# Optimization experiments

Hardware: AMD Instinct MI355X
Metric: run time of the kernel (lower is better)

## Reference

```python
import jax, jax.numpy as jnp
import numpy as np

N, E, F_IN, H = 10000, 20000, 128, 8
C1, C2 = 512, 256          # per-head channels: head_dim1*8, head_dim2*8
B, OUT = 64, 10            # graphs per batch, output_dim


def _lin(k, fi, fo):
    return (jax.random.normal(k, (fi, fo), jnp.float32) / np.sqrt(fi)).astype(jnp.float32)


def setup_inputs() -> dict:
    key = jax.random.key(0)
    ks = jax.random.split(key, 24)
    inp = {
        "x": jax.random.normal(ks[0], (N, F_IN), jnp.float32),
        "edge_index": jax.random.randint(ks[1], (2, E), 0, N),
        "batch": jnp.sort(jax.random.randint(ks[2], (N,), 0, B)),
        # conv1 (in=F_IN, per-head C1, H heads)
        "Wq1": _lin(ks[3], F_IN, H * C1), "bq1": 0.01 * jax.random.normal(ks[4], (H * C1,)),
        "Wk1": _lin(ks[5], F_IN, H * C1), "bk1": 0.01 * jax.random.normal(ks[6], (H * C1,)),
        "Wv1": _lin(ks[7], F_IN, H * C1), "bv1": 0.01 * jax.random.normal(ks[8], (H * C1,)),
        "Ws1": _lin(ks[9], F_IN, C1), "bs1": 0.01 * jax.random.normal(ks[10], (C1,)),
        # conv2 (in=C1, per-head C2)
        "Wq2": _lin(ks[11], C1, H * C2), "bq2": 0.01 * jax.random.normal(ks[12], (H * C2,)),
        "Wk2": _lin(ks[13], C1, H * C2), "bk2": 0.01 * jax.random.normal(ks[14], (H * C2,)),
        "Wv2": _lin(ks[15], C1, H * C2), "bv2": 0.01 * jax.random.normal(ks[16], (H * C2,)),
        "Ws2": _lin(ks[17], C1, C2), "bs2": 0.01 * jax.random.normal(ks[18], (C2,)),
        # GlobalAttention gate and final fc
        "Wg": _lin(ks[19], C2, 1), "bg": jnp.zeros((1,), jnp.float32),
        "Wf": _lin(ks[20], C2, OUT), "bf": 0.01 * jax.random.normal(ks[21], (OUT,)),
    }
    return inp


def _segment_softmax(alpha, idx, n):
    # numerically-stable softmax over variable-size segments (PyG softmax)
    amax = jax.ops.segment_max(alpha, idx, num_segments=n)
    amax = jnp.where(jnp.isfinite(amax), amax, 0.0)
    e = jnp.exp(alpha - amax[idx])
    denom = jax.ops.segment_sum(e, idx, num_segments=n)
    return e / (denom[idx] + 1e-16)


def _transformer_conv(x, edge_index, Wq, bq, Wk, bk, Wv, bv, Ws, bs, C):
    n = x.shape[0]
    src, dst = edge_index[0], edge_index[1]  # message flows src -> dst
    q = (x @ Wq + bq).reshape(n, H, C)
    k = (x @ Wk + bk).reshape(n, H, C)
    v = (x @ Wv + bv).reshape(n, H, C)
    # per-edge multi-head attention logits [E, H]
    alpha = jnp.einsum('ehc,ehc->eh', q[dst], k[src]) / np.sqrt(C).astype(np.float32)
    a = _segment_softmax(alpha, dst, n)                       # [E, H]
    out = jax.ops.segment_sum(a[:, :, None] * v[src], dst, num_segments=n)  # [N, H, C]
    out = out.mean(axis=1)                                    # concat=False -> head mean
    return out + x @ Ws + bs                                  # root/skip connection


def reference(x, edge_index, batch,
              Wq1, bq1, Wk1, bk1, Wv1, bv1, Ws1, bs1,
              Wq2, bq2, Wk2, bk2, Wv2, bv2, Ws2, bs2,
              Wg, bg, Wf, bf):
    h = jax.nn.elu(_transformer_conv(x, edge_index, Wq1, bq1, Wk1, bk1, Wv1, bv1, Ws1, bs1, C1))
    h = jax.nn.elu(_transformer_conv(h, edge_index, Wq2, bq2, Wk2, bk2, Wv2, bv2, Ws2, bs2, C2))
    # GlobalAttention pooling: gate softmax within each graph, weighted sum
    gate = _segment_softmax((h @ Wg + bg)[:, 0], batch, B)    # [N]
    g = jax.ops.segment_sum(gate[:, None] * h, batch, num_segments=B)  # [B, C2]
    return g @ Wf + bf
```

## Files before the change

### kernel.cpp

```cpp
#include <hip/hip_runtime.h>
#include <math.h>

#define NN 10000
#define NE 20000
#define FIN 128
#define NHEAD 8
#define C1 512
#define C2 256
#define NB 64
#define NOUT 10

typedef _Float16 half8v __attribute__((ext_vector_type(8)));
typedef _Float16 half4v __attribute__((ext_vector_type(4)));
typedef _Float16 half2v __attribute__((ext_vector_type(2)));
typedef float f32x4 __attribute__((ext_vector_type(4)));

template<int VEC> struct VecT;
template<> struct VecT<2> { using T = half2v; };
template<> struct VecT<4> { using T = half4v; };
template<> struct VecT<8> { using T = half8v; };

__device__ __forceinline__ unsigned enc_f(float f) {
    unsigned u = __float_as_uint(f);
    return (u & 0x80000000u) ? ~u : (u | 0x80000000u);
}
__device__ __forceinline__ float dec_f(unsigned e) {
    return (e & 0x80000000u) ? __uint_as_float(e & 0x7fffffffu) : __uint_as_float(~e);
}

__device__ __forceinline__ void gload16(const _Float16* g, _Float16* l) {
    __builtin_amdgcn_global_load_lds(
        (const __attribute__((address_space(1))) unsigned int*)(const void*)g,
        (__attribute__((address_space(3))) unsigned int*)(void*)l, 16, 0, 0);
}

__device__ __forceinline__ void swz_map(int nwg, int gx, int SW, int& bx, int& by) {
    int orig = blockIdx.x;
    int q = nwg >> 3, r = nwg & 7;
    int xcd = orig & 7, lid = orig >> 3;
    int wgid = (xcd < r ? xcd * (q + 1) : r * (q + 1) + (xcd - r) * q) + lid;
    int gy = nwg / gx;
    int sh = SW * gy;
    int stripe = wgid / sh;
    int rem = wgid - stripe * sh;
    int byq = rem / SW;
    by = byq;
    bx = stripe * SW + (rem - byq * SW);
}

__global__ void cvt_f16(const float* __restrict__ in, _Float16* __restrict__ out, int n) {
    int i = blockIdx.x * blockDim.x + threadIdx.x;
    if (i < n) out[i] = (_Float16)in[i];
}

__global__ void transpose_cvt(const float* __restrict__ W, _Float16* __restrict__ Wt,
                              int K, int N) {
    __shared__ float tile[32][33];
    int n0 = blockIdx.x * 32, k0 = blockIdx.y * 32;
    int tx = threadIdx.x, ty = threadIdx.y;
    for (int j = ty; j < 32; j += 8) tile[j][tx] = W[(size_t)(k0 + j) * N + n0 + tx];
    __syncthreads();
    for (int j = ty; j < 32; j += 8)
        Wt[(size_t)(n0 + j) * K + k0 + tx] = (_Float16)tile[tx][j];
}

__global__ void transpose_stack(const float* __restrict__ Wv, _Float16* __restrict__ Bt,
                                int Cin, int Cout) {
    __shared__ float tile[32][33];
    int h = blockIdx.z;
    int c0 = blockIdx.x * 32, k0 = blockIdx.y * 32;
    int tx = threadIdx.x, ty = threadIdx.y;
    for (int j = ty; j < 32; j += 8)
        tile[j][tx] = Wv[(size_t)(k0 + j) * (NHEAD * Cout) + (size_t)h * Cout + c0 + tx];
    __syncthreads();
    for (int j = ty; j < 32; j += 8)
        Bt[(size_t)(c0 + j) * (NHEAD * Cin) + (size_t)h * Cin + k0 + tx] = (_Float16)tile[tx][j];
}

__global__ void bvmean_k(const float* __restrict__ bv, float* __restrict__ bvm, int C) {
    int c = blockIdx.x * blockDim.x + threadIdx.x;
    if (c >= C) return;
    float s = 0.f;
    #pragma unroll
    for (int h = 0; h < NHEAD; ++h) s += bv[h * C + c];
    bvm[c] = s * (1.0f / NHEAD);
}

__global__ void bcat2_k(const float* __restrict__ bq2, const float* __restrict__ bk2,
                        const float* __restrict__ bv2, const float* __restrict__ bs2,
                        float* __restrict__ o) {
    int i = blockIdx.x * blockDim.x + threadIdx.x;
    const int n = NHEAD * C2;
    if (i < n) o[i] = bq2[i];
    else if (i < 2 * n) o[i] = bk2[i - n];
    else if (i < 3 * n) o[i] = bv2[i - 2 * n];
    else if (i < 3 * n + C2) o[i] = bs2[i - 3 * n];
}

__global__ void mstack_k(const _Float16* __restrict__ wtq1, const _Float16* __restrict__ wtk1,
                         _Float16* __restrict__ Mst) {
    int h = blockIdx.z;
    int i = blockIdx.x * 16 + threadIdx.x;
    int j = blockIdx.y * 16 + threadIdx.y;
    float acc = 0.f;
    for (int c = 0; c < C1; ++c)
        acc += (float)wtq1[((size_t)h * C1 + c) * FIN + i] *
               (float)wtk1[((size_t)h * C1 + c) * FIN + j];
    Mst[((size_t)h * FIN + j) * FIN + i] = (_Float16)acc;
}

__global__ void uvprep_w(const float* __restrict__ Wq1, const float* __restrict__ Wk1,
                         const float* __restrict__ bq1, const float* __restrict__ bk1,
                         float* __restrict__ u, float* __restrict__ v) {
    int wid = (blockIdx.x * blockDim.x + threadIdx.x) >> 6;
    int lane = threadIdx.x & 63;
    if (wid >= NHEAD * FIN) return;
    int h = wid >> 7, i = wid & 127;
    const float* wq = Wq1 + (size_t)i * (NHEAD * C1) + h * C1;
    const float* wk = Wk1 + (size_t)i * (NHEAD * C1) + h * C1;
    const float* bk = bk1 + h * C1;
    const float* bq = bq1 + h * C1;
    int c = lane * 8;
    float4 a0 = *(const float4*)(wq + c),  a1 = *(const float4*)(wq + c + 4);
    float4 p0 = *(const float4*)(bk + c),  p1 = *(const float4*)(bk + c + 4);
    float4 b0 = *(const float4*)(wk + c),  b1 = *(const float4*)(wk + c + 4);
    float4 q0 = *(const float4*)(bq + c),  q1 = *(const float4*)(bq + c + 4);
    float su = a0.x*p0.x + a0.y*p0.y + a0.z*p0.z + a0.w*p0.w
             + a1.x*p1.x + a1.y*p1.y + a1.z*p1.z + a1.w*p1.w;
    float sv = b0.x*q0.x + b0.y*q0.y + b0.z*q0.z + b0.w*q0.w
             + b1.x*q1.x + b1.y*q1.y + b1.z*q1.z + b1.w*q1.w;
    #pragma unroll
    for (int off = 32; off; off >>= 1) {
        su += __shfl_xor(su, off);
        sv += __shfl_xor(sv, off);
    }
    if (lane == 0) { u[h * FIN + i] = su; v[h * FIN + i] = sv; }
}

__global__ void chd_k(const float* __restrict__ bq1, const float* __restrict__ bk1,
                      float* __restrict__ ch) {
    int h = threadIdx.x >> 6, lane = threadIdx.x & 63;
    int c = lane * 8;
    const float* bq = bq1 + h * C1;
    const float* bk = bk1 + h * C1;
    float4 a0 = *(const float4*)(bq + c), a1 = *(const float4*)(bq + c + 4);
    float4 b0 = *(const float4*)(bk + c), b1 = *(const float4*)(bk + c + 4);
    float s = a0.x*b0.x + a0.y*b0.y + a0.z*b0.z + a0.w*b0.w
            + a1.x*b1.x + a1.y*b1.y + a1.z*b1.z + a1.w*b1.w;
    #pragma unroll
    for (int off = 32; off; off >>= 1) s += __shfl_xor(s, off);
    if (lane == 0) ch[h] = s;
}

__global__ void udvs_w(const _Float16* __restrict__ xb, const float* __restrict__ u,
                       const float* __restrict__ v, const float* __restrict__ ch,
                       float* __restrict__ ud, float* __restrict__ vs) {
    int n = (blockIdx.x * blockDim.x + threadIdx.x) >> 6;
    int lane = threadIdx.x & 63;
    if (n >= NN) return;
    half2v xv = *(const half2v*)(xb + (size_t)n * FIN + lane * 2);
    float x0 = (float)xv[0], x1 = (float)xv[1];
    #pragma unroll
    for (int h = 0; h < NHEAD; ++h) {
        float2 uu = *(const float2*)(u + h * FIN + lane * 2);
        float2 vv = *(const float2*)(v + h * FIN + lane * 2);
        float su = x0 * uu.x + x1 * uu.y;
        float sv = x0 * vv.x + x1 * vv.y;
        #pragma unroll
        for (int off = 32; off; off >>= 1) {
            su += __shfl_xor(su, off);
            sv += __shfl_xor(sv, off);
        }
        if (lane == 0) {
            ud[(size_t)n * NHEAD + h] = su + ch[h];
            vs[(size_t)n * NHEAD + h] = sv;
        }
    }
}

#define GEMM_CORE                                                                   \
    __shared__ _Float16 As[128 * 32];                                               \
    __shared__ _Float16 Bs[128 * 32];                                               \
    __shared__ _Float16 Ct[64 * 136];                                               \
    const int t = threadIdx.x;                                                      \
    const int w = t >> 6, lane = t & 63;                                            \
    const int wr = w >> 1, wc = w & 1;                                              \
    const int r_lo = lane >> 2, slot = lane & 3;                                    \
    f32x4 acc[4][4];                                                                \
    _Pragma("unroll")                                                               \
    for (int m = 0; m < 4; ++m)                                                     \
        _Pragma("unroll")                                                           \
        for (int n = 0; n < 4; ++n)                                                 \
            _Pragma("unroll")                                                       \
            for (int j = 0; j < 4; ++j) acc[m][n][j] = 0.f;

#define GEMM_STEP(APTR, ALD, AKO, BPTR, BLD, BKO)                                   \
    {                                                                               \
        _Pragma("unroll")                                                           \
        for (int i = 0; i < 2; ++i) {                                               \
            int chunk = 2 * w + i;                                                  \
            int row = chunk * 16 + r_lo;                                            \
            int gr = m0 + row; gr = gr < M ? gr : M - 1;                            \
            gload16(APTR + (size_t)gr * ALD + AKO + slot * 8, &As[chunk * 512]);    \
            gload16(BPTR + (size_t)(n0 + row) * BLD + BKO + slot * 8, &Bs[chunk * 512]); \
        }                                                                           \
        __syncthreads();                                                            \
        half8v af[4], bf[4];                                                        \
        _Pragma("unroll")                                                           \
        for (int m = 0; m < 4; ++m)                                                 \
            af[m] = *(const half8v*)(&As[(wr * 64 + m * 16 + (lane & 15)) * 32 + (lane >> 4) * 8]); \
        _Pragma("unroll")                                                           \
        for (int n = 0; n < 4; ++n)                                                 \
            bf[n] = *(const half8v*)(&Bs[(wc * 64 + n * 16 + (lane & 15)) * 32 + (lane >> 4) * 8]); \
        _Pragma("unroll")                                                           \
        for (int m = 0; m < 4; ++m)                                                 \
            _Pragma("unroll")                                                       \
            for (int n = 0; n < 4; ++n)                                             \
                acc[m][n] = __builtin_amdgcn_mfma_f32_16x16x32_f16(af[m], bf[n], acc[m][n], 0, 0, 0); \
        __syncthreads();                                                            \
    }

#define EPI_F16(OUTPTR, LDC, STAGE_EXPR)                                            \
    _Pragma("unroll")                                                               \
    for (int half = 0; half < 2; ++half) {                                          \
        __syncthreads();                                                            \
        if (wr == half) {                                                           \
            _Pragma("unroll")                                                       \
            for (int m = 0; m < 4; ++m)                                             \
                _Pragma("unroll")                                                   \
                for (int n = 0; n < 4; ++n) {                                       \
                    int lcol = wc * 64 + n * 16 + (lane & 15);                      \
                    int gcol = n0 + lcol;                                           \
                    _Pragma("unroll")                                               \
                    for (int r = 0; r < 4; ++r) {                                   \
                        int lrow = m * 16 + (lane >> 4) * 4 + r;                    \
                        int grow = m0 + half * 64 + lrow;                           \
                        float av = acc[m][n][r];                                    \
                        Ct[lrow * 136 + lcol] = (_Float16)(STAGE_EXPR);             \
                    }                                                               \
                }                                                                   \
        }                                                                           \
        __syncthreads();                                                            \
        _Pragma("unroll")                                                           \
        for (int g = 0; g < 4; ++g) {                                               \
            int lrow = g * 16 + (t >> 4);                                           \
            int grow = m0 + half * 64 + lrow;                                       \
            if (grow < M) {                                                         \
                int seg = (t & 15) * 8;                                             \
                *(float4*)(OUTPTR + (size_t)grow * LDC + n0 + seg) =                \
                    *(const float4*)(&Ct[lrow * 136 + seg]);                        \
            }                                                                       \
        }                                                                           \
    }

__global__ __launch_bounds__(256) void gemm_f16(
    const _Float16* __restrict__ A, const _Float16* __restrict__ Bt,
    const float* __restrict__ bias, _Float16* __restrict__ Cout, int ldc,
    int M, int K, int nwg, int gx, int SW)
{
    int bx, by; swz_map(nwg, gx, SW, bx, by);
    const int m0 = by * 128, n0 = bx * 128;
    GEMM_CORE
    for (int k0 = 0; k0 < K; k0 += 32) GEMM_STEP(A, K, k0, Bt, K, k0)
    EPI_F16(Cout, ldc, av + bias[gcol])
}

__global__ __launch_bounds__(256) void gemm_dual(
    const _Float16* __restrict__ A, const _Float16* __restrict__ Bt,
    const float* __restrict__ bias, _Float16* __restrict__ out16, int ld16,
    float* __restrict__ out32, int ld32, int NSPLIT, int M, int K,
    int nwg, int gx, int SW)
{
    int bx, by; swz_map(nwg, gx, SW, bx, by);
    const int m0 = by * 128, n0 = bx * 128;
    GEMM_CORE
    for (int k0 = 0; k0 < K; k0 += 32) GEMM_STEP(A, K, k0, Bt, K, k0)
    if (n0 < NSPLIT) {
        EPI_F16(out16, ld16, av + bias[gcol])
    } else {
        #pragma unroll
        for (int m = 0; m < 4; ++m) {
            int r0 = m0 + wr * 64 + m * 16 + (lane >> 4) * 4;
            #pragma unroll
            for (int n = 0; n < 4; ++n) {
                int col = n0 + wc * 64 + n * 16 + (lane & 15);
                float b = bias[col];
                #pragma unroll
                for (int r = 0; r < 4; ++r) {
                    int row = r0 + r;
                    if (row < M)
                        out32[(size_t)row * ld32 + (col - NSPLIT)] = acc[m][n][r] + b;
                }
            }
        }
    }
}

__global__ __launch_bounds__(256) void gemm_cat2_elu(
    const _Float16* __restrict__ A1, int K1, const _Float16* __restrict__ A2, int K2,
    const _Float16* __restrict__ B1, const _Float16* __restrict__ B2,
    const float* __restrict__ bs1, const float* __restrict__ bvm1,
    const int* __restrict__ deg, _Float16* __restrict__ h1b,
    int M, int nwg, int gx, int SW)
{
    int bx, by; swz_map(nwg, gx, SW, bx, by);
    const int m0 = by * 128, n0 = bx * 128;
    const int K = K1 + K2;
    GEMM_CORE
    for (int k0 = 0; k0 < K; k0 += 32) {
        if (k0 < K1) GEMM_STEP(A1, K1, k0, B1, K1, k0)
        else         GEMM_STEP(A2, K2, (k0 - K1), B2, K2, (k0 - K1))
    }
    EPI_F16(h1b, C1,
        ({ int dr = grow < M ? grow : M - 1;
           float vv = av + bs1[gcol] + (deg[dr] > 0 ? bvm1[gcol] : 0.f);
           vv > 0.f ? vv : expm1f(vv); }))
}

__global__ void zero_i32(int* __restrict__ p, int n) {
    int i = blockIdx.x * blockDim.x + threadIdx.x;
    if (i < n) p[i] = 0;
}
__global__ void hist_dst(const int* __restrict__ dst, int* __restrict__ deg) {
    int e = blockIdx.x * blockDim.x + threadIdx.x;
    if (e < NE) atomicAdd(&deg[dst[e]], 1);
}
__global__ void scan_deg(const int* __restrict__ deg, int* __restrict__ rowptr,
                         int* __restrict__ cursor, int n) {
    __shared__ int s[256];
    __shared__ int carry;
    int t = threadIdx.x;
    if (t == 0) carry = 0;
    __syncthreads();
    for (int base = 0; base < n; base += 256) {
        int v = (base + t < n) ? deg[base + t] : 0;
        s[t] = v;
        __syncthreads();
        for (int off = 1; off < 256; off <<= 1) {
            int x = (t >= off) ? s[t - off] : 0;
            __syncthreads();
            s[t] += x;
            __syncthreads();
        }
        int excl = carry + s[t] - v;
        if (base + t < n) { rowptr[base + t] = excl; cursor[base + t] = excl; }
        __syncthreads();
        if (t == 255) carry += s[255];
        __syncthreads();
    }
    if (t == 0) rowptr[n] = carry;
}
__global__ void scatter_edges(const int* __restrict__ dst, int* __restrict__ cursor,
                              int* __restrict__ eids) {
    int e = blockIdx.x * blockDim.x + threadIdx.x;
    if (e < NE) {
        int pos = atomicAdd(&cursor[dst[e]], 1);
        eids[pos] = e;
    }
}

__global__ void init_seg(unsigned* __restrict__ amax, float* __restrict__ denom, int n) {
    int i = blockIdx.x * blockDim.x + threadIdx.x;
    if (i < n) { amax[i] = 0x007FFFFFu; denom[i] = 0.f; }
}

__global__ void edge_alpha_lr(const _Float16* __restrict__ T, const _Float16* __restrict__ X,
                              const float* __restrict__ ud, const float* __restrict__ vs,
                              const int* __restrict__ src, const int* __restrict__ dst,
                              float* __restrict__ alpha, unsigned* __restrict__ amaxU,
                              float scale)
{
    int gi = blockIdx.x * blockDim.x + threadIdx.x;
    int e = gi >> 6, lane = threadIdx.x & 63;
    if (e >= NE) return;
    int s = src[e], d = dst[e];
    half2v xv = *(const half2v*)(X + (size_t)s * FIN + lane * 2);
    #pragma unroll
    for (int h = 0; h < NHEAD; ++h) {
        half2v tv = *(const half2v*)(T + ((size_t)d * NHEAD + h) * FIN + lane * 2);
        float sum = (float)tv[0] * (float)xv[0] + (float)tv[1] * (float)xv[1];
        #pragma unroll
        for (int off = 32; off; off >>= 1) sum += __shfl_xor(sum, off);
        if (lane == 0) {
            float al = (sum + ud[(size_t)d * NHEAD + h] + vs[(size_t)s * NHEAD + h]) * scale;
            alpha[(size_t)e * NHEAD + h] = al;
            atomicMax(&amaxU[(size_t)d * NHEAD + h], enc_f(al));
        }
    }
}

template<int C, int G>
__global__ void edge_alpha_fu(const _Float16* __restrict__ Q, const _Float16* __restrict__ Kh,
                              int ldq, const int* __restrict__ src, const int* __restrict__ dst,
                              float* __restrict__ alpha, unsigned* __restrict__ amaxU,
                              float scale)
{
    constexpr int VEC = C / 64;
    using vecH = typename VecT<VEC>::T;
    int gi = blockIdx.x * blockDim.x + threadIdx.x;
    int e = gi >> 6, lane = threadIdx.x & 63;
    if (e >= NE) return;
    int s = src[e], d = dst[e];
    const _Float16* qp = Q + (size_t)d * ldq + lane * VEC;
    const _Float16* kp = Kh + (size_t)s * ldq + lane * VEC;
    vecH q[G], k[G];
    #pragma unroll
    for (int h = 0; h < G; ++h) {
        q[h] = *(const vecH*)(qp + h * C);
        k[h] = *(const vecH*)(kp + h * C);
    }
    #pragma unroll
    for (int h = 0; h < G; ++h) {
        float sum = 0.f;
        #pragma unroll
        for (int j = 0; j < VEC; ++j) sum += (float)q[h][j] * (float)k[h][j];
        #pragma unroll
        for (int off = 32; off; off >>= 1) sum += __shfl_xor(sum, off);
        if (lane == 0) {
            float al = sum * scale;
            alpha[(size_t)e * NHEAD + h] = al;
            atomicMax(&amaxU[(size_t)d * NHEAD + h], enc_f(al));
        }
    }
}

__global__ void edge_expsum(const float* __restrict__ alpha, const int* __restrict__ dst,
                            const unsigned* __restrict__ amaxU,
                            float* __restrict__ ev, float* __restrict__ denom)
{
    int i = blockIdx.x * blockDim.x + threadIdx.x;
    if (i >= NE * NHEAD) return;
    int e = i >> 3, h = i & 7;
    int d = dst[e];
    float ex = expf(alpha[i] - dec_f(amaxU[(size_t)d * NHEAD + h]));
    ev[i] = ex;
    atomicAdd(&denom[(size_t)d * NHEAD + h], ex);
}

template<int C, int G>
__global__ void zaccum(const _Float16* __restrict__ X, const float* __restrict__ ev,
                       const float* __restrict__ denom, const int* __restrict__ rowptr,
                       const int* __restrict__ eids, const int* __restrict__ src,
                       _Float16* __restrict__ Z, int hbase)
{
    constexpr int VEC = C / 64;
    using vecH = typename VecT<VEC>::T;
    int gi = blockIdx.x * blockDim.x + threadIdx.x;
    int n = gi >> 6, lane = threadIdx.x & 63;
    if (n >= NN) return;
    int beg = rowptr[n], end = rowptr[n + 1];
    float rd[G];
    #pragma unroll
    for (int h = 0; h < G; ++h)
        rd[h] = (1.0f / NHEAD) / (denom[(size_t)n * NHEAD + hbase + h] + 1e-16f);
    float acc[G][VEC];
    #pragma unroll
    for (int h = 0; h < G; ++h)
        #pragma unroll
        for (int j = 0; j < VEC; ++j) acc[h][j] = 0.f;
    for (int i = beg; i < end; ++i) {
        int e = eids[i];
        int s = src[e];
        vecH xv = *(const vecH*)(X + (size_t)s * C + lane * VEC);
        #pragma unroll
        for (int h = 0; h < G; ++h) {
            float cf = ev[(size_t)e * NHEAD + hbase + h] * rd[h];
            #pragma unroll
            for (int j = 0; j < VEC; ++j) acc[h][j] += cf * (float)xv[j];
        }
    }
    #pragma unroll
    for (int h = 0; h < G; ++h) {
        vecH o;
        #pragma unroll
        for (int j = 0; j < VEC; ++j) o[j] = (_Float16)acc[h][j];
        *(vecH*)(Z + (size_t)n * (G * C) + (size_t)h * C + lane * VEC) = o;
    }
}

template<int C, int G>
__global__ void node_aggr_ilp(const _Float16* __restrict__ V, int ldv,
                              const float* __restrict__ ev, const float* __restrict__ denom,
                              const int* __restrict__ rowptr, const int* __restrict__ eids,
                              const int* __restrict__ src, float* __restrict__ acc)
{
    constexpr int VEC = C / 64;
    using vecH = typename VecT<VEC>::T;
    int gi = blockIdx.x * blockDim.x + threadIdx.x;
    int n = gi >> 6, lane = threadIdx.x & 63;
    if (n >= NN) return;
    int beg = rowptr[n], end = rowptr[n + 1];
    float rd[G];
    #pragma unroll
    for (int h = 0; h < G; ++h)
        rd[h] = (1.0f / NHEAD) / (denom[(size_t)n * NHEAD + h] + 1e-16f);
    float a[VEC];
    #pragma unroll
    for (int j = 0; j < VEC; ++j) a[j] = 0.f;
    for (int i = beg; i < end; ++i) {
        int e = eids[i];
        int s = src[e];
        float cf[G];
        #pragma unroll
        for (int h = 0; h < G; ++h) cf[h] = ev[(size_t)e * NHEAD + h] * rd[h];
        vecH v[G];
        #pragma unroll
        for (int h = 0; h < G; ++h)
            v[h] = *(const vecH*)(V + (size_t)s * ldv + h * C + lane * VEC);
        #pragma unroll
        for (int h = 0; h < G; ++h)
            #pragma unroll
            for (int j = 0; j < VEC; ++j) a[j] += cf[h] * (float)v[h][j];
    }
    float* ap = acc + (size_t)n * C + lane * VEC;
    #pragma unroll
    for (int j = 0; j < VEC; ++j) ap[j] += a[j];
}

__global__ void elu_k(float* __restrict__ x, int n) {
    int i = blockIdx.x * blockDim.x + threadIdx.x;
    if (i < n) { float v = x[i]; x[i] = v > 0.f ? v : expm1f(v); }
}

__global__ __launch_bounds__(256) void pool_fused(
    const float* __restrict__ H2, const float* __restrict__ Wg,
    const float* __restrict__ bg, const int* __restrict__ batch,
    const float* __restrict__ Wf, const float* __restrict__ bf,
    float* __restrict__ glogit, float* __restrict__ out)
{
    const int b = blockIdx.x;
    const int t = threadIdx.x, lane = t & 63, w = t >> 6;
    __shared__ int sbeg, send;
    __shared__ float sred[4];
    if (t == 0) {
        int lo = 0, hi = NN;
        while (lo < hi) { int mid = (lo + hi) >> 1; if (batch[mid] < b) lo = mid + 1; else hi = mid; }
        sbeg = lo;
        hi = NN;
        while (lo < hi) { int mid = (lo + hi) >> 1; if (batch[mid] < b + 1) lo = mid + 1; else hi = mid; }
        send = lo;
    }
    __syncthreads();
    const int beg = sbeg, end = send;
    const float bg0 = bg[0];

    float lmax = -INFINITY;
    for (int n = beg + w; n < end; n += 4) {
        float4 h = ((const float4*)(H2 + (size_t)n * C2))[lane];
        float4 wv = ((const float4*)Wg)[lane];
        float sum = h.x * wv.x + h.y * wv.y + h.z * wv.z + h.w * wv.w;
        #pragma unroll
        for (int off = 32; off; off >>= 1) sum += __shfl_xor(sum, off);
        sum += bg0;
        if (lane == 0) glogit[n] = sum;
        lmax = fmaxf(lmax, sum);
    }
    if (lane == 0) sred[w] = lmax;
    __syncthreads();
    float m = fmaxf(fmaxf(sred[0], sred[1]), fmaxf(sred[2], sred[3]));
    if (!isfinite(m)) m = 0.f;
    __syncthreads();

    float ls = 0.f;
    for (int n = beg + t; n < end; n += 256) {
        float e = expf(glogit[n] - m);
        glogit[n] = e;
        ls += e;
    }
    #pragma unroll
    for (int off = 32; off; off >>= 1) ls += __shfl_xor(ls, off);
    if (lane == 0) sred[w] = ls;
    __syncthreads();
    const float denom = sred[0] + sred[1] + sred[2] + sred[3] + 1e-16f;
    __syncthreads();

    float acc = 0.f;
    for (int n = beg; n < end; ++n)
        acc += glogit[n] * H2[(size_t)n * C2 + t];
    const float gc = acc / denom;

    for (int o = 0; o < NOUT; ++o) {
        float p = gc * Wf[t * NOUT + o];
        #pragma unroll
        for (int off = 32; off; off >>= 1) p += __shfl_xor(p, off);
        __syncthreads();
        if (lane == 0) sred[w] = p;
        __syncthreads();
        if (t == 0) out[b * NOUT + o] = sred[0] + sred[1] + sred[2] + sred[3] + bf[o];
    }
}

extern "C" void kernel_launch(void* const* d_in, const int* in_sizes, int n_in,
                              void* d_out, int out_size, void* d_ws, size_t ws_size,
                              hipStream_t stream) {
    (void)in_sizes; (void)n_in; (void)out_size; (void)ws_size;
    const float* x     = (const float*)d_in[0];
    const int*   ei    = (const int*)  d_in[1];
    const int*   batch = (const int*)  d_in[2];
    const float* Wq1 = (const float*)d_in[3];  const float* bq1 = (const float*)d_in[4];
    const float* Wk1 = (const float*)d_in[5];  const float* bk1 = (const float*)d_in[6];
    const float* Wv1 = (const float*)d_in[7];  const float* bv1 = (const float*)d_in[8];
    const float* Ws1 = (const float*)d_in[9];  const float* bs1 = (const float*)d_in[10];
    const float* Wq2 = (const float*)d_in[11]; const float* bq2 = (const float*)d_in[12];
    const float* Wk2 = (const float*)d_in[13]; const float* bk2 = (const float*)d_in[14];
    const float* Wv2 = (const float*)d_in[15]; const float* bv2 = (const float*)d_in[16];
    const float* Ws2 = (const float*)d_in[17]; const float* bs2 = (const float*)d_in[18];
    const float* Wg  = (const float*)d_in[19]; const float* bg  = (const float*)d_in[20];
    const float* Wf  = (const float*)d_in[21]; const float* bf  = (const float*)d_in[22];

    const int* src = ei;
    const int* dst = ei + NE;

    char* base = (char*)d_ws;
    size_t off = 0;
    auto alloc = [&](size_t bytes) -> char* {
        char* p = base + off;
        off = (off + bytes + 255) & ~(size_t)255;
        return p;
    };
    _Float16* xb    = (_Float16*)alloc((size_t)NN * FIN * 2);
    _Float16* wtq1  = (_Float16*)alloc((size_t)NHEAD * C1 * FIN * 2);
    _Float16* wtk1  = (_Float16*)alloc((size_t)NHEAD * C1 * FIN * 2);
    _Float16* bvs1  = (_Float16*)alloc((size_t)C1 * NHEAD * FIN * 2);
    _Float16* wts1  = (_Float16*)alloc((size_t)C1 * FIN * 2);
    _Float16* Mst   = (_Float16*)alloc((size_t)NHEAD * FIN * FIN * 2);
    _Float16* wcat2 = (_Float16*)alloc((size_t)(3 * NHEAD * C2 + C2) * C1 * 2);
    float* uvecs = (float*)alloc((size_t)NHEAD * FIN * 4);
    float* vvecs = (float*)alloc((size_t)NHEAD * FIN * 4);
    float* chd   = (float*)alloc((size_t)NHEAD * 4);
    float* ud    = (float*)alloc((size_t)NN * NHEAD * 4);
    float* vs    = (float*)alloc((size_t)NN * NHEAD * 4);
    float* zbias = (float*)alloc((size_t)NHEAD * FIN * 4);
    float* bcat2 = (float*)alloc((size_t)(3 * NHEAD * C2 + C2) * 4);
    float* acc2  = (float*)alloc((size_t)NN * C2 * 4);
    _Float16* h1b = (_Float16*)alloc((size_t)NN * C1 * 2);
    float* alpha = (float*)alloc((size_t)NE * NHEAD * 4);
    float* ev    = (float*)alloc((size_t)NE * NHEAD * 4);
    unsigned* amaxU = (unsigned*)alloc((size_t)NN * NHEAD * 4);
    float* denom = (float*)alloc((size_t)NN * NHEAD * 4);
    int* deg    = (int*)alloc((size_t)NN * 4);
    int* rowptr = (int*)alloc((size_t)(NN + 1) * 4);
    int* cursor = (int*)alloc((size_t)NN * 4);
    int* eids   = (int*)alloc((size_t)NE * 4);
    float* bvm1 = (float*)alloc((size_t)C1 * 4);
    _Float16* Tbuf   = (_Float16*)alloc((size_t)NN * NHEAD * FIN * 2);
    _Float16* QKVbuf = (_Float16*)alloc((size_t)NN * 3 * NHEAD * C2 * 2);
    _Float16* Zbuf = QKVbuf;
    const int LDQKV = 3 * NHEAD * C2;

    _Float16* wq2t = wcat2;
    _Float16* wk2t = wcat2 + (size_t)NHEAD * C2 * C1;
    _Float16* wv2t = wcat2 + (size_t)2 * NHEAD * C2 * C1;
    _Float16* ws2t = wcat2 + (size_t)3 * NHEAD * C2 * C1;

    const dim3 blk(256);
    const float sc1 = 1.0f / sqrtf((float)C1);
    const float sc2 = 1.0f / sqrtf((float)C2);
    const int edge_blocks = (NE * 64) / 256;
    const int node_blocks = (NN * 64) / 256;
    const int gy = (NN + 127) / 128;

    cvt_f16<<<((size_t)NN * FIN + 255) / 256, blk, 0, stream>>>(x, xb, NN * FIN);
    {
        dim3 tb(32, 8);
        transpose_cvt<<<dim3(NHEAD * C1 / 32, FIN / 32), tb, 0, stream>>>(Wq1, wtq1, FIN, NHEAD * C1);
        transpose_cvt<<<dim3(NHEAD * C1 / 32, FIN / 32), tb, 0, stream>>>(Wk1, wtk1, FIN, NHEAD * C1);
        transpose_stack<<<dim3(C1 / 32, FIN / 32, NHEAD), tb, 0, stream>>>(Wv1, bvs1, FIN, C1);
        transpose_cvt<<<dim3(C1 / 32, FIN / 32),         tb, 0, stream>>>(Ws1, wts1, FIN, C1);
        transpose_cvt<<<dim3(NHEAD * C2 / 32, C1 / 32),  tb, 0, stream>>>(Wq2, wq2t, C1, NHEAD * C2);
        transpose_cvt<<<dim3(NHEAD * C2 / 32, C1 / 32),  tb, 0, stream>>>(Wk2, wk2t, C1, NHEAD * C2);
        transpose_cvt<<<dim3(NHEAD * C2 / 32, C1 / 32),  tb, 0, stream>>>(Wv2, wv2t, C1, NHEAD * C2);
        transpose_cvt<<<dim3(C2 / 32, C1 / 32),          tb, 0, stream>>>(Ws2, ws2t, C1, C2);
    }
    bvmean_k<<<(C1 + 255) / 256, blk, 0, stream>>>(bv1, bvm1, C1);
    mstack_k<<<dim3(FIN / 16, FIN / 16, NHEAD), dim3(16, 16), 0, stream>>>(wtq1, wtk1, Mst);
    uvprep_w<<<(NHEAD * FIN * 64) / 256, blk, 0, stream>>>(Wq1, Wk1, bq1, bk1, uvecs, vvecs);
    chd_k<<<1, 512, 0, stream>>>(bq1, bk1, chd);
    udvs_w<<<node_blocks, blk, 0, stream>>>(xb, uvecs, vvecs, chd, ud, vs);
    zero_i32<<<(NHEAD * FIN + 255) / 256, blk, 0, stream>>>((int*)zbias, NHEAD * FIN);
    bcat2_k<<<(3 * NHEAD * C2 + C2 + 255) / 256, blk, 0, stream>>>(bq2, bk2, bv2, bs2, bcat2);

    zero_i32<<<(NN + 255) / 256, blk, 0, stream>>>(deg, NN);
    hist_dst<<<(NE + 255) / 256, blk, 0, stream>>>(dst, deg);
    scan_deg<<<1, blk, 0, stream>>>(deg, rowptr, cursor, NN);
    scatter_edges<<<(NE + 255) / 256, blk, 0, stream>>>(dst, cursor, eids);

    {
        int nwg = 8 * gy;
        gemm_f16<<<nwg, blk, 0, stream>>>(xb, Mst, zbias, Tbuf, NHEAD * FIN, NN, FIN,
                                          nwg, 8, 8);
    }
    init_seg<<<(NN * NHEAD + 255) / 256, blk, 0, stream>>>(amaxU, denom, NN * NHEAD);
    edge_alpha_lr<<<edge_blocks, blk, 0, stream>>>(Tbuf, xb, ud, vs, src, dst,
                                                   alpha, amaxU, sc1);
    edge_expsum<<<(NE * NHEAD + 255) / 256, blk, 0, stream>>>(alpha, dst, amaxU, ev, denom);
    zaccum<FIN, NHEAD><<<node_blocks, blk, 0, stream>>>(xb, ev, denom, rowptr, eids, src,
                                                        Zbuf, 0);
    {
        int nwg = 4 * gy;
        gemm_cat2_elu<<<nwg, blk, 0, stream>>>(Zbuf, NHEAD * FIN, xb, FIN,
                                               bvs1, wts1, bs1, bvm1, deg, h1b,
                                               NN, nwg, 4, 4);
    }

    init_seg<<<(NN * NHEAD + 255) / 256, blk, 0, stream>>>(amaxU, denom, NN * NHEAD);
    {
        int nwg = 50 * gy;
        gemm_dual<<<nwg, blk, 0, stream>>>(h1b, wcat2, bcat2, QKVbuf, LDQKV,
                                           acc2, C2, LDQKV, NN, C1, nwg, 50, 25);
    }
    edge_alpha_fu<C2, NHEAD><<<edge_blocks, blk, 0, stream>>>(
        QKVbuf, QKVbuf + NHEAD * C2, LDQKV, src, dst, alpha, amaxU, sc2);
    edge_expsum<<<(NE * NHEAD + 255) / 256, blk, 0, stream>>>(alpha, dst, amaxU, ev, denom);
    node_aggr_ilp<C2, NHEAD><<<node_blocks, blk, 0, stream>>>(
        QKVbuf + 2 * NHEAD * C2, LDQKV, ev, denom, rowptr, eids, src, acc2);
    elu_k<<<((size_t)NN * C2 + 255) / 256, blk, 0, stream>>>(acc2, NN * C2);

    pool_fused<<<NB, blk, 0, stream>>>(acc2, Wg, bg, batch, Wf, bf, alpha, (float*)d_out);
}
```

Before: 585.6 us.

## Double-buffer GEMM shared-memory tiles to overlap global loads with MFMA

Replaces the single-buffered load-sync-compute-sync GEMM loop with a two-stage ping-pong pipeline across all three GEMM kernels. The next K-slice's async global-to-LDS loads are issued before computing the current slice, with explicit vmcnt waits and s_barrier calls. This aims to hide global memory latency behind MFMA work, at the cost of more LDS per block, which may lower occupancy, and reliance on hand-tuned waitcnt counts. The epilogue staging buffer now aliases the first pipeline buffer.

```diff
diff --git a/kernel.cpp b/kernel.cpp
--- a/kernel.cpp
+++ b/kernel.cpp
@@ -179,9 +179,8 @@
 }
 
 #define GEMM_CORE                                                                   \
-    __shared__ _Float16 As[128 * 32];                                               \
-    __shared__ _Float16 Bs[128 * 32];                                               \
-    __shared__ _Float16 Ct[64 * 136];                                               \
+    __shared__ _Float16 SM[4][128 * 32];                                            \
+    _Float16* Ct = &SM[0][0];                       \
     const int t = threadIdx.x;                                                      \
     const int w = t >> 6, lane = t & 63;                                            \
     const int wr = w >> 1, wc = w & 1;                                              \
@@ -194,31 +193,48 @@
             _Pragma("unroll")                                                       \
             for (int j = 0; j < 4; ++j) acc[m][n][j] = 0.f;
 
-#define GEMM_STEP(APTR, ALD, AKO, BPTR, BLD, BKO)                                   \
+#define GEMM_STAGE(BUF, APTR, ALD, AKO, BPTR, BLD, BKO)                             \
     {                                                                               \
         _Pragma("unroll")                                                           \
         for (int i = 0; i < 2; ++i) {                                               \
             int chunk = 2 * w + i;                                                  \
             int row = chunk * 16 + r_lo;                                            \
             int gr = m0 + row; gr = gr < M ? gr : M - 1;                            \
-            gload16(APTR + (size_t)gr * ALD + AKO + slot * 8, &As[chunk * 512]);    \
-            gload16(BPTR + (size_t)(n0 + row) * BLD + BKO + slot * 8, &Bs[chunk * 512]); \
+            gload16(APTR + (size_t)gr * ALD + (AKO) + slot * 8, &SM[(BUF)*2+0][chunk * 512]); \
+            gload16(BPTR + (size_t)(n0 + row) * BLD + (BKO) + slot * 8, &SM[(BUF)*2+1][chunk * 512]); \
         }                                                                           \
-        __syncthreads();                                                            \
+    }
+
+#define GEMM_COMPUTE(BUF)                                                           \
+    {                                                                               \
         half8v af[4], bf[4];                                                        \
         _Pragma("unroll")                                                           \
         for (int m = 0; m < 4; ++m)                                                 \
-            af[m] = *(const half8v*)(&As[(wr * 64 + m * 16 + (lane & 15)) * 32 + (lane >> 4) * 8]); \
+            af[m] = *(const half8v*)(&SM[(BUF)*2+0][(wr * 64 + m * 16 + (lane & 15)) * 32 + (lane >> 4) * 8]); \
         _Pragma("unroll")                                                           \
         for (int n = 0; n < 4; ++n)                                                 \
-            bf[n] = *(const half8v*)(&Bs[(wc * 64 + n * 16 + (lane & 15)) * 32 + (lane >> 4) * 8]); \
+            bf[n] = *(const half8v*)(&SM[(BUF)*2+1][(wc * 64 + n * 16 + (lane & 15)) * 32 + (lane >> 4) * 8]); \
         _Pragma("unroll")                                                           \
         for (int m = 0; m < 4; ++m)                                                 \
             _Pragma("unroll")                                                       \
             for (int n = 0; n < 4; ++n)                                             \
                 acc[m][n] = __builtin_amdgcn_mfma_f32_16x16x32_f16(af[m], bf[n], acc[m][n], 0, 0, 0); \
-        __syncthreads();                                                            \
-    }
+    }
+
+#define PIPE_WAIT_PREV                                                              \
+    asm volatile("s_waitcnt vmcnt(4)" ::: "memory");                                \
+    __builtin_amdgcn_sched_barrier(0);                                              \
+    __builtin_amdgcn_s_barrier();                                                   \
+    __builtin_amdgcn_sched_barrier(0);
+#define PIPE_WAIT_ALL                                                               \
+    asm volatile("s_waitcnt vmcnt(0)" ::: "memory");                                \
+    __builtin_amdgcn_sched_barrier(0);                                              \
+    __builtin_amdgcn_s_barrier();                                                   \
+    __builtin_amdgcn_sched_barrier(0);
+#define PIPE_END                                                                    \
+    __builtin_amdgcn_sched_barrier(0);                                              \
+    __builtin_amdgcn_s_barrier();                                                   \
+    __builtin_amdgcn_sched_barrier(0);
 
 #define EPI_F16(OUTPTR, LDC, STAGE_EXPR)                                            \
     _Pragma("unroll")                                                               \
@@ -261,7 +277,21 @@
     int bx, by; swz_map(nwg, gx, SW, bx, by);
     const int m0 = by * 128, n0 = bx * 128;
     GEMM_CORE
-    for (int k0 = 0; k0 < K; k0 += 32) GEMM_STEP(A, K, k0, Bt, K, k0)
+    GEMM_STAGE(0, A, K, 0, Bt, K, 0)
+    int cur = 0;
+    const int nsteps = K >> 5;
+    for (int s = 0; s < nsteps; ++s) {
+        if (s + 1 < nsteps) {
+            int ko = (s + 1) << 5;
+            GEMM_STAGE(cur ^ 1, A, K, ko, Bt, K, ko)
+            PIPE_WAIT_PREV
+        } else {
+            PIPE_WAIT_ALL
+        }
+        GEMM_COMPUTE(cur)
+        PIPE_END
+        cur ^= 1;
+    }
     EPI_F16(Cout, ldc, av + bias[gcol])
 }
 
@@ -274,7 +304,21 @@
     int bx, by; swz_map(nwg, gx, SW, bx, by);
     const int m0 = by * 128, n0 = bx * 128;
     GEMM_CORE
-    for (int k0 = 0; k0 < K; k0 += 32) GEMM_STEP(A, K, k0, Bt, K, k0)
+    GEMM_STAGE(0, A, K, 0, Bt, K, 0)
+    int cur = 0;
+    const int nsteps = K >> 5;
+    for (int s = 0; s < nsteps; ++s) {
+        if (s + 1 < nsteps) {
+            int ko = (s + 1) << 5;
+            GEMM_STAGE(cur ^ 1, A, K, ko, Bt, K, ko)
+            PIPE_WAIT_PREV
+        } else {
+            PIPE_WAIT_ALL
+        }
+        GEMM_COMPUTE(cur)
+        PIPE_END
+        cur ^= 1;
+    }
     if (n0 < NSPLIT) {
         EPI_F16(out16, ld16, av + bias[gcol])
     } else {
@@ -305,11 +349,28 @@
 {
     int bx, by; swz_map(nwg, gx, SW, bx, by);
     const int m0 = by * 128, n0 = bx * 128;
-    const int K = K1 + K2;
     GEMM_CORE
-    for (int k0 = 0; k0 < K; k0 += 32) {
-        if (k0 < K1) GEMM_STEP(A1, K1, k0, B1, K1, k0)
-        else         GEMM_STEP(A2, K2, (k0 - K1), B2, K2, (k0 - K1))
+    GEMM_STAGE(0, A1, K1, 0, B1, K1, 0)
+    int cur = 0;
+    const int nsteps = (K1 + K2) >> 5;
+    const int split = K1 >> 5;
+    for (int s = 0; s < nsteps; ++s) {
+        if (s + 1 < nsteps) {
+            int sn = s + 1;
+            if (sn < split) {
+                int ko = sn << 5;
+                GEMM_STAGE(cur ^ 1, A1, K1, ko, B1, K1, ko)
+            } else {
+                int ko = (sn - split) << 5;
+                GEMM_STAGE(cur ^ 1, A2, K2, ko, B2, K2, ko)
+            }
+            PIPE_WAIT_PREV
+        } else {
+            PIPE_WAIT_ALL
+        }
+        GEMM_COMPUTE(cur)
+        PIPE_END
+        cur ^= 1;
     }
     EPI_F16(h1b, C1,
         ({ int dr = grow < M ? grow : M - 1;
```

Result: faster. 552.3 us (-5.7%).
